# Kernel tuning notes

Measured on AMD Instinct MI355X. Metric: run time of the kernel, lower is better.

The kernel has to match this reference:

```python
import jax, jax.numpy as jnp
import numpy as np

B, S, D, H = 2, 2048, 1024, 16
DEPTH = D // H


def setup_inputs() -> dict:
    key = jax.random.key(0)
    ks = jax.random.split(key, 11)
    s = 1.0 / np.sqrt(D)
    return {
        "Q": jax.random.normal(ks[0], (B, S, D), jnp.float32),
        "K": jax.random.normal(ks[1], (B, S, D), jnp.float32),
        "V": jax.random.normal(ks[2], (B, S, D), jnp.float32),
        "wq": jax.random.normal(ks[3], (D, D), jnp.float32) * s,
        "bq": jnp.zeros((D,), jnp.float32),
        "wk": jax.random.normal(ks[4], (D, D), jnp.float32) * s,
        "bk": jnp.zeros((D,), jnp.float32),
        "wv": jax.random.normal(ks[5], (D, D), jnp.float32) * s,
        "bv": jnp.zeros((D,), jnp.float32),
        "wo": jax.random.normal(ks[6], (D, D), jnp.float32) * s,
        "bo": jnp.zeros((D,), jnp.float32),
    }


def _split_heads(x):
    # [B, S, D] -> [B, H, S, depth]
    b, s, _ = x.shape
    return x.reshape(b, s, H, DEPTH).transpose(0, 2, 1, 3)


def reference(Q, K, V, wq, bq, wk, bk, wv, bv, wo, bo):
    q = _split_heads(Q @ wq + bq)
    k = _split_heads(K @ wk + bk)
    v = _split_heads(V @ wv + bv)
    scores = jnp.einsum("bhqd,bhkd->bhqk", q, k) / jnp.sqrt(jnp.float32(DEPTH))
    weights = jax.nn.softmax(scores, axis=-1)
    attn = jnp.einsum("bhqk,bhkd->bhqd", weights, v)
    concat = attn.transpose(0, 2, 1, 3).reshape(Q.shape[0], -1, D)
    out = concat @ wo + bo
    return out, weights
```

## Files before the change

kernel.cpp:

```cpp
#include <hip/hip_runtime.h>
#include <stdint.h>


typedef _Float16 half8 __attribute__((ext_vector_type(8)));
typedef float f32x4 __attribute__((ext_vector_type(4)));

#define MFMA16(a, b, c) __builtin_amdgcn_mfma_f32_16x16x32_f16((a), (b), (c), 0, 0, 0)

__device__ __forceinline__ void load_lds16(const void* g, void* l) {
  __builtin_amdgcn_global_load_lds(
      (const __attribute__((address_space(1))) void*)(uintptr_t)g,
      (__attribute__((address_space(3))) void*)(uintptr_t)l, 16, 0, 0);
}

__global__ __launch_bounds__(256) void cvt_f16_kernel(
    const float* __restrict__ i0, const float* __restrict__ i1,
    const float* __restrict__ i2, _Float16* __restrict__ o0,
    _Float16* __restrict__ o1, _Float16* __restrict__ o2) {
  const float* in;
  _Float16* out;
  switch (blockIdx.y) {
    case 0: in = i0; out = o0; break;
    case 1: in = i1; out = o1; break;
    default: in = i2; out = o2; break;
  }
  const int i = blockIdx.x * 256 + threadIdx.x;
  const float4* p = (const float4*)in + 2 * (size_t)i;
  float4 a = p[0], b = p[1];
  half8 h;
  h[0] = (_Float16)a.x; h[1] = (_Float16)a.y; h[2] = (_Float16)a.z; h[3] = (_Float16)a.w;
  h[4] = (_Float16)b.x; h[5] = (_Float16)b.y; h[6] = (_Float16)b.z; h[7] = (_Float16)b.w;
  *((half8*)out + i) = h;
}

__global__ __launch_bounds__(256) void transpose_cvt_kernel(
    const float* __restrict__ i0, const float* __restrict__ i1,
    const float* __restrict__ i2, const float* __restrict__ i3,
    _Float16* __restrict__ o0, _Float16* __restrict__ o1,
    _Float16* __restrict__ o2, _Float16* __restrict__ o3) {
  const float* in;
  _Float16* out;
  switch (blockIdx.z) {
    case 0: in = i0; out = o0; break;
    case 1: in = i1; out = o1; break;
    case 2: in = i2; out = o2; break;
    default: in = i3; out = o3; break;
  }
  __shared__ _Float16 tile[64][72];
  const int r  = threadIdx.x >> 2;
  const int c4 = threadIdx.x & 3;
  const int kin = blockIdx.y * 64, nin = blockIdx.x * 64;
#pragma unroll
  for (int i = 0; i < 4; ++i) {
    float4 v = *(const float4*)(in + (size_t)(kin + r) * 1024 + nin + c4 * 16 + i * 4);
    tile[c4 * 16 + i * 4 + 0][r] = (_Float16)v.x;
    tile[c4 * 16 + i * 4 + 1][r] = (_Float16)v.y;
    tile[c4 * 16 + i * 4 + 2][r] = (_Float16)v.z;
    tile[c4 * 16 + i * 4 + 3][r] = (_Float16)v.w;
  }
  __syncthreads();
#pragma unroll
  for (int i = 0; i < 4; ++i) {
    union { _Float16 hh[4]; uint2 u; } p;
    p.hh[0] = tile[r][c4 * 16 + i * 4 + 0];
    p.hh[1] = tile[r][c4 * 16 + i * 4 + 1];
    p.hh[2] = tile[r][c4 * 16 + i * 4 + 2];
    p.hh[3] = tile[r][c4 * 16 + i * 4 + 3];
    *(uint2*)(out + (size_t)(nin + r) * 1024 + kin + c4 * 16 + i * 4) = p.u;
  }
}

struct GemmArgs {
  const _Float16* A[3];
  const _Float16* BT[3];
  const float* bias[3];
  void* out[3];
};

__global__ __launch_bounds__(256, 3) void gemm_f16_kernel(GemmArgs ga, int K,
                                                          int modes) {
  const _Float16* __restrict__ A  = ga.A[blockIdx.z];
  const _Float16* __restrict__ BT = ga.BT[blockIdx.z];
  const float* __restrict__ bias  = ga.bias[blockIdx.z];
  void* __restrict__ out          = ga.out[blockIdx.z];
  const int MODE = (modes >> (4 * blockIdx.z)) & 15;

  __shared__ __align__(16) _Float16 As[128 * 32];
  __shared__ __align__(16) _Float16 Bs[128 * 32];
  const int tid = threadIdx.x;
  const int w = tid >> 6, l = tid & 63;
  const int g = l >> 4, c = l & 15;
  const int tm = blockIdx.y * 128, tn = blockIdx.x * 128;
  const int wr = w >> 1, wc = w & 1;

  f32x4 acc[4][4];
#pragma unroll
  for (int i = 0; i < 4; ++i)
#pragma unroll
    for (int j = 0; j < 4; ++j) acc[i][j] = (f32x4){0.f, 0.f, 0.f, 0.f};

  const int srow0 = w * 16 + (l >> 2);
  const int sl = l & 3;

  for (int kt = 0; kt < K; kt += 32) {
#pragma unroll
    for (int r = 0; r < 2; ++r) {
      const int row = r * 64 + srow0;
      const int kc = sl ^ ((row >> 1) & 3);
      load_lds16(A + (size_t)(tm + row) * K + kt + kc * 8, As + row * 32 + sl * 8);
      load_lds16(BT + (size_t)(tn + row) * K + kt + kc * 8, Bs + row * 32 + sl * 8);
    }
    __syncthreads();
    half8 af[4], bf[4];
#pragma unroll
    for (int mt = 0; mt < 4; ++mt) {
      const int row = wr * 64 + mt * 16 + c;
      af[mt] = *(const half8*)(As + row * 32 + (g ^ ((row >> 1) & 3)) * 8);
    }
#pragma unroll
    for (int nt = 0; nt < 4; ++nt) {
      const int row = wc * 64 + nt * 16 + c;
      bf[nt] = *(const half8*)(Bs + row * 32 + (g ^ ((row >> 1) & 3)) * 8);
    }
#pragma unroll
    for (int mt = 0; mt < 4; ++mt)
#pragma unroll
      for (int nt = 0; nt < 4; ++nt)
        acc[mt][nt] = MFMA16(af[mt], bf[nt], acc[mt][nt]);
    __syncthreads();
  }

#pragma unroll
  for (int mt = 0; mt < 4; ++mt) {
#pragma unroll
    for (int nt = 0; nt < 4; ++nt) {
      const int n = tn + wc * 64 + nt * 16 + c;
      const float bv = bias[n];
      if (MODE == 2) {
#pragma unroll
        for (int r = 0; r < 4; ++r) {
          const int m = tm + wr * 64 + mt * 16 + 4 * g + r;
          ((float*)out)[(size_t)m * 1024 + n] = acc[mt][nt][r] + bv;
        }
      } else if (MODE == 0) {
        const int h_ = n >> 6, d_ = n & 63;
#pragma unroll
        for (int r = 0; r < 4; ++r) {
          const int m = tm + wr * 64 + mt * 16 + 4 * g + r;
          const int b_ = m >> 11, s_ = m & 2047;
          ((_Float16*)out)[((size_t)(b_ * 16 + h_) * 2048 + s_) * 64 + d_] =
              (_Float16)(acc[mt][nt][r] + bv);
        }
      } else {
        const int h_ = n >> 6, d_ = n & 63;
        const int m0 = tm + wr * 64 + mt * 16 + 4 * g;
        const int b_ = m0 >> 11, s0 = m0 & 2047;
        union { _Float16 hh[4]; uint2 u; } p;
#pragma unroll
        for (int r = 0; r < 4; ++r) p.hh[r] = (_Float16)(acc[mt][nt][r] + bv);
        *(uint2*)((_Float16*)out + ((size_t)(b_ * 16 + h_) * 64 + d_) * 2048 + s0) = p.u;
      }
    }
  }
}

__global__ __launch_bounds__(256, 2) void pv_kernel(
    const _Float16* __restrict__ qh,
    const _Float16* __restrict__ kh,
    const _Float16* __restrict__ vT,
    float* __restrict__ invp,
    _Float16* __restrict__ concat) {
  __shared__ __align__(16) char arena[32768];
  _Float16* Kb0 = (_Float16*)(arena);
  _Float16* Kb1 = (_Float16*)(arena + 8192);
  _Float16* Vb0 = (_Float16*)(arena + 16384);
  _Float16* Vb1 = (_Float16*)(arena + 24576);

  const int tid = threadIdx.x;
  const int w = tid >> 6, l = tid & 63;
  const int g = l >> 4, c = l & 15;
  const int qt = blockIdx.x, h = blockIdx.y, b = blockIdx.z;
  const int bh = b * 16 + h;
  const int q0 = qt * 128 + w * 32;
  const _Float16* qp = qh + ((size_t)bh * 2048 + q0) * 64;
  const _Float16* kp = kh + (size_t)bh * 2048 * 64;
  const _Float16* vp = vT + (size_t)bh * 64 * 2048;

  const half8 aq00 = *(const half8*)(qp + (size_t)c * 64 + 8 * g);
  const half8 aq01 = *(const half8*)(qp + (size_t)c * 64 + 32 + 8 * g);
  const half8 aq10 = *(const half8*)(qp + (size_t)(16 + c) * 64 + 8 * g);
  const half8 aq11 = *(const half8*)(qp + (size_t)(16 + c) * 64 + 32 + 8 * g);

  f32x4 pvA0 = {0,0,0,0}, pvA1 = {0,0,0,0}, pvA2 = {0,0,0,0}, pvA3 = {0,0,0,0};
  f32x4 pvB0 = {0,0,0,0}, pvB1 = {0,0,0,0}, pvB2 = {0,0,0,0}, pvB3 = {0,0,0,0};
  float sum0 = 0.f, sum1 = 0.f;

  const int L01 = (2 * (g & 1)) * 16 + c;
  const int L23 = L01 + 16;
  const bool lohalf = (g < 2);

  const int n0 = tid, n1 = tid + 256;
  const int r0 = n0 >> 3, s0 = n0 & 7, z0 = (s0 ^ (r0 & 7)) * 8;
  const int r1 = n1 >> 3, s1 = n1 & 7, z1 = (s1 ^ (r1 & 7)) * 8;

#define STAGE_PV(Kb, Vb, kc)                                                 \
  do {                                                                       \
    load_lds16(kp + (size_t)((kc) + r0) * 64 + z0, (Kb) + n0 * 8);           \
    load_lds16(kp + (size_t)((kc) + r1) * 64 + z1, (Kb) + n1 * 8);           \
    load_lds16(vp + (size_t)r0 * 2048 + (kc) + z0, (Vb) + n0 * 8);           \
    load_lds16(vp + (size_t)r1 * 2048 + (kc) + z1, (Vb) + n1 * 8);           \
  } while (0)

  STAGE_PV(Kb0, Vb0, 0);
  __syncthreads();

#pragma unroll 1
  for (int ch = 0; ch < 32; ++ch) {
    const int cur = ch & 1;
    const _Float16* Kb = cur ? Kb1 : Kb0;
    const _Float16* Vb = cur ? Vb1 : Vb0;
    if (ch < 31) {
      if (cur) STAGE_PV(Kb0, Vb0, (ch + 1) * 64);
      else     STAGE_PV(Kb1, Vb1, (ch + 1) * 64);
    }

    float e0[16], e1[16];
#pragma unroll
    for (int t = 0; t < 4; ++t) {
      const int krow = t * 16 + c;
      const int swz = krow & 7;
      half8 k0 = *(const half8*)(Kb + krow * 64 + ((g ^ swz) * 8));
      half8 k1 = *(const half8*)(Kb + krow * 64 + (((4 + g) ^ swz) * 8));
      f32x4 sA = {0.f, 0.f, 0.f, 0.f}, sB = {0.f, 0.f, 0.f, 0.f};
      sA = MFMA16(k0, aq00, sA);
      sA = MFMA16(k1, aq01, sA);
      sB = MFMA16(k0, aq10, sB);
      sB = MFMA16(k1, aq11, sB);
#pragma unroll
      for (int r = 0; r < 4; ++r) {
        e0[t * 4 + r] = __expf(sA[r] * 0.125f);
        sum0 += e0[t * 4 + r];
        e1[t * 4 + r] = __expf(sB[r] * 0.125f);
        sum1 += e1[t * 4 + r];
      }
    }

#pragma unroll
    for (int kh2 = 0; kh2 < 2; ++kh2) {
      const int d0 = 0 * 16 + c, d1 = 1 * 16 + c, d2 = 2 * 16 + c, d3 = 3 * 16 + c;
      half8 v0 = *(const half8*)(Vb + d0 * 64 + (((kh2 * 4 + g) ^ (d0 & 7)) * 8));
      half8 v1 = *(const half8*)(Vb + d1 * 64 + (((kh2 * 4 + g) ^ (d1 & 7)) * 8));
      half8 v2 = *(const half8*)(Vb + d2 * 64 + (((kh2 * 4 + g) ^ (d2 & 7)) * 8));
      half8 v3 = *(const half8*)(Vb + d3 * 64 + (((kh2 * 4 + g) ^ (d3 & 7)) * 8));

      {
        union { _Float16 h2[2]; unsigned u; } p0, p1, p2, p3;
        p0.h2[0] = (_Float16)e0[kh2*8+0]; p0.h2[1] = (_Float16)e0[kh2*8+1];
        p1.h2[0] = (_Float16)e0[kh2*8+2]; p1.h2[1] = (_Float16)e0[kh2*8+3];
        p2.h2[0] = (_Float16)e0[kh2*8+4]; p2.h2[1] = (_Float16)e0[kh2*8+5];
        p3.h2[0] = (_Float16)e0[kh2*8+6]; p3.h2[1] = (_Float16)e0[kh2*8+7];
        unsigned s0a = __shfl(p0.u, L01, 64), s0b = __shfl(p2.u, L01, 64);
        unsigned s1a = __shfl(p1.u, L01, 64), s1b = __shfl(p3.u, L01, 64);
        unsigned s2a = __shfl(p0.u, L23, 64), s2b = __shfl(p2.u, L23, 64);
        unsigned s3a = __shfl(p1.u, L23, 64), s3b = __shfl(p3.u, L23, 64);
        union { unsigned u[4]; half8 h; } aw;
        aw.u[0] = lohalf ? s0a : s0b;
        aw.u[1] = lohalf ? s1a : s1b;
        aw.u[2] = lohalf ? s2a : s2b;
        aw.u[3] = lohalf ? s3a : s3b;
        pvA0 = MFMA16(aw.h, v0, pvA0);
        pvA1 = MFMA16(aw.h, v1, pvA1);
        pvA2 = MFMA16(aw.h, v2, pvA2);
        pvA3 = MFMA16(aw.h, v3, pvA3);
      }
      {
        union { _Float16 h2[2]; unsigned u; } p0, p1, p2, p3;
        p0.h2[0] = (_Float16)e1[kh2*8+0]; p0.h2[1] = (_Float16)e1[kh2*8+1];
        p1.h2[0] = (_Float16)e1[kh2*8+2]; p1.h2[1] = (_Float16)e1[kh2*8+3];
        p2.h2[0] = (_Float16)e1[kh2*8+4]; p2.h2[1] = (_Float16)e1[kh2*8+5];
        p3.h2[0] = (_Float16)e1[kh2*8+6]; p3.h2[1] = (_Float16)e1[kh2*8+7];
        unsigned s0a = __shfl(p0.u, L01, 64), s0b = __shfl(p2.u, L01, 64);
        unsigned s1a = __shfl(p1.u, L01, 64), s1b = __shfl(p3.u, L01, 64);
        unsigned s2a = __shfl(p0.u, L23, 64), s2b = __shfl(p2.u, L23, 64);
        unsigned s3a = __shfl(p1.u, L23, 64), s3b = __shfl(p3.u, L23, 64);
        union { unsigned u[4]; half8 h; } aw;
        aw.u[0] = lohalf ? s0a : s0b;
        aw.u[1] = lohalf ? s1a : s1b;
        aw.u[2] = lohalf ? s2a : s2b;
        aw.u[3] = lohalf ? s3a : s3b;
        pvB0 = MFMA16(aw.h, v0, pvB0);
        pvB1 = MFMA16(aw.h, v1, pvB1);
        pvB2 = MFMA16(aw.h, v2, pvB2);
        pvB3 = MFMA16(aw.h, v3, pvB3);
      }
    }
    __syncthreads();
  }
#undef STAGE_PV

  sum0 += __shfl_xor(sum0, 16, 64);
  sum0 += __shfl_xor(sum0, 32, 64);
  sum1 += __shfl_xor(sum1, 16, 64);
  sum1 += __shfl_xor(sum1, 32, 64);
  const float inv0 = 1.0f / sum0;
  const float inv1 = 1.0f / sum1;
  if (l < 16) {
    invp[(size_t)bh * 2048 + q0 + l] = inv0;
    invp[(size_t)bh * 2048 + q0 + 16 + l] = inv1;
  }
  float ivA[4], ivB[4];
#pragma unroll
  for (int r = 0; r < 4; ++r) {
    ivA[r] = __shfl(inv0, 4 * g + r, 64);
    ivB[r] = __shfl(inv1, 4 * g + r, 64);
  }

  float* part = (float*)arena + w * (16 * 68);
  const int ql = l & 15, dh2 = l >> 4;
#pragma unroll
  for (int qs = 0; qs < 2; ++qs) {
    const f32x4* s0p = qs ? &pvB0 : &pvA0;
    const f32x4* s1p = qs ? &pvB1 : &pvA1;
    const f32x4* s2p = qs ? &pvB2 : &pvA2;
    const f32x4* s3p = qs ? &pvB3 : &pvA3;
    const float* iv = qs ? ivB : ivA;
#pragma unroll
    for (int r = 0; r < 4; ++r) {
      part[(4 * g + r) * 68 + 0 * 16 + c] = (*s0p)[r] * iv[r];
      part[(4 * g + r) * 68 + 1 * 16 + c] = (*s1p)[r] * iv[r];
      part[(4 * g + r) * 68 + 2 * 16 + c] = (*s2p)[r] * iv[r];
      part[(4 * g + r) * 68 + 3 * 16 + c] = (*s3p)[r] * iv[r];
    }
    __builtin_amdgcn_s_waitcnt(0);
    union { _Float16 hh[8]; uint4 u4; } pk;
#pragma unroll
    for (int half = 0; half < 2; ++half) {
#pragma unroll
      for (int i = 0; i < 8; ++i)
        pk.hh[i] = (_Float16)part[ql * 68 + dh2 * 16 + half * 8 + i];
      *(uint4*)(concat + (size_t)(b * 2048 + q0 + qs * 16 + ql) * 1024 +
                h * 64 + dh2 * 16 + half * 8) = pk.u4;
    }
  }
}

__global__ __launch_bounds__(256, 2) void wts_kernel(
    const _Float16* __restrict__ qh, const _Float16* __restrict__ kh,
    const float* __restrict__ invp, float* __restrict__ wout) {
  __shared__ __align__(16) _Float16 Qs[128 * 64];
  __shared__ __align__(16) _Float16 Ks[128 * 64];
  __shared__ __align__(16) float stg[4][16][132];
  __shared__ float invs[128];
  const int tid = threadIdx.x;
  const int w = tid >> 6, l = tid & 63;
  const int g = l >> 4, c = l & 15;
  const int tk = blockIdx.x * 128, tq = blockIdx.y * 128;
  const int bh = blockIdx.z;
  const _Float16* qg = qh + ((size_t)bh * 2048 + tq) * 64;
  const _Float16* kg = kh + ((size_t)bh * 2048 + tk) * 64;

  if (tid < 128) invs[tid] = invp[(size_t)bh * 2048 + tq + tid];

#pragma unroll
  for (int rnd = 0; rnd < 4; ++rnd) {
    const int seg = w * 4 + rnd;
    const int row = seg * 8 + (l >> 3);
    const int ss = (l & 7) ^ (row & 7);
    load_lds16(qg + (size_t)row * 64 + ss * 8, Qs + seg * 512 + l * 8);
    load_lds16(kg + (size_t)row * 64 + ss * 8, Ks + seg * 512 + l * 8);
  }
  __syncthreads();

  half8 af[2][2];
#pragma unroll
  for (int mt = 0; mt < 2; ++mt) {
#pragma unroll
    for (int dh = 0; dh < 2; ++dh) {
      const int row = w * 32 + mt * 16 + c;
      af[mt][dh] = *(const half8*)(Qs + row * 64 + (((dh * 4 + g) ^ (row & 7)) * 8));
    }
  }

  f32x4 acc[2][8];
#pragma unroll
  for (int mt = 0; mt < 2; ++mt)
#pragma unroll
    for (int nt = 0; nt < 8; ++nt) acc[mt][nt] = (f32x4){0.f, 0.f, 0.f, 0.f};

#pragma unroll
  for (int nt = 0; nt < 8; ++nt) {
    const int row = nt * 16 + c;
    half8 bf0 = *(const half8*)(Ks + row * 64 + ((g ^ (row & 7)) * 8));
    half8 bf1 = *(const half8*)(Ks + row * 64 + (((4 + g) ^ (row & 7)) * 8));
    acc[0][nt] = MFMA16(af[0][0], bf0, acc[0][nt]);
    acc[0][nt] = MFMA16(af[0][1], bf1, acc[0][nt]);
    acc[1][nt] = MFMA16(af[1][0], bf0, acc[1][nt]);
    acc[1][nt] = MFMA16(af[1][1], bf1, acc[1][nt]);
  }

#pragma unroll
  for (int hs = 0; hs < 2; ++hs) {
#pragma unroll
    for (int r = 0; r < 4; ++r) {
      const float iv = invs[w * 32 + hs * 16 + 4 * g + r];
#pragma unroll
      for (int nt = 0; nt < 8; ++nt)
        stg[w][4 * g + r][nt * 16 + c] = __expf(acc[hs][nt][r] * 0.125f) * iv;
    }
    asm volatile("s_waitcnt lgkmcnt(0)" ::: "memory");
#pragma unroll
    for (int i = 0; i < 8; ++i) {
      const int idx = i * 64 + l;
      const int row = idx >> 5, col4 = idx & 31;
      f32x4 v = *(const f32x4*)(&stg[w][row][col4 * 4]);
      __builtin_nontemporal_store(
          v, (f32x4*)(wout + ((size_t)bh * 2048 + tq + w * 32 + hs * 16 + row) *
                                 2048 + tk) + col4);
    }
  }
}

extern "C" void kernel_launch(void* const* d_in, const int* in_sizes, int n_in,
                              void* d_out, int out_size, void* d_ws, size_t ws_size,
                              hipStream_t stream) {
  const float* Q  = (const float*)d_in[0];
  const float* Kx = (const float*)d_in[1];
  const float* V  = (const float*)d_in[2];
  const float* wq = (const float*)d_in[3];
  const float* bq = (const float*)d_in[4];
  const float* wk = (const float*)d_in[5];
  const float* bk = (const float*)d_in[6];
  const float* wv = (const float*)d_in[7];
  const float* bv = (const float*)d_in[8];
  const float* wo = (const float*)d_in[9];
  const float* bo = (const float*)d_in[10];

  float* out  = (float*)d_out;
  float* wout = out + (size_t)4194304;

  char* ws = (char*)d_ws;
  const size_t MB = 1024 * 1024;
  _Float16* Xq  = (_Float16*)(ws + 0 * MB);
  _Float16* Xk  = (_Float16*)(ws + 8 * MB);
  _Float16* Xv  = (_Float16*)(ws + 16 * MB);
  _Float16* wqT = (_Float16*)(ws + 24 * MB);
  _Float16* wkT = (_Float16*)(ws + 26 * MB);
  _Float16* wvT = (_Float16*)(ws + 28 * MB);
  _Float16* woT = (_Float16*)(ws + 30 * MB);
  _Float16* qhp = (_Float16*)(ws + 32 * MB);
  _Float16* khp = (_Float16*)(ws + 40 * MB);
  _Float16* vTp = (_Float16*)(ws + 48 * MB);
  _Float16* cat = (_Float16*)(ws + 56 * MB);
  float*    invp = (float*)(ws + 16 * MB);

  cvt_f16_kernel<<<dim3(2048, 3), 256, 0, stream>>>(Q, Kx, V, Xq, Xk, Xv);
  transpose_cvt_kernel<<<dim3(16, 16, 4), 256, 0, stream>>>(
      wq, wk, wv, wo, wqT, wkT, wvT, woT);

  GemmArgs qkv;
  qkv.A[0] = Xq;  qkv.A[1] = Xk;  qkv.A[2] = Xv;
  qkv.BT[0] = wqT; qkv.BT[1] = wkT; qkv.BT[2] = wvT;
  qkv.bias[0] = bq; qkv.bias[1] = bk; qkv.bias[2] = bv;
  qkv.out[0] = qhp; qkv.out[1] = khp; qkv.out[2] = vTp;
  gemm_f16_kernel<<<dim3(8, 32, 3), 256, 0, stream>>>(qkv, 1024, 0x100);

  pv_kernel<<<dim3(16, 16, 2), 256, 0, stream>>>(qhp, khp, vTp, invp, cat);
  wts_kernel<<<dim3(16, 16, 32), 256, 0, stream>>>(qhp, khp, invp, wout);

  GemmArgs og;
  og.A[0] = cat; og.A[1] = cat; og.A[2] = cat;
  og.BT[0] = woT; og.BT[1] = woT; og.BT[2] = woT;
  og.bias[0] = bo; og.bias[1] = bo; og.bias[2] = bo;
  og.out[0] = out; og.out[1] = out; og.out[2] = out;
  gemm_f16_kernel<<<dim3(8, 32, 1), 256, 0, stream>>>(og, 1024, 0x2);
}
```

Baseline: 241.5 us.

## Merge prologue conversions and fuse output projection into weights kernel launch

Merges the activation f16 conversion and the weight transpose-conversion into one prologue launch. It also folds the output-projection GEMM into the attention-weights kernel as an extra z-slice of blocks sharing one LDS arena. The goal is to cut launch overhead and let the output GEMM overlap with the large weights-writing work instead of running as a serialized tail. In exchange, both block types in the fused kernel share one LDS footprint and occupancy limit, which may constrain the GEMM blocks.

```diff
diff --git a/kernel.cpp b/kernel.cpp
--- a/kernel.cpp
+++ b/kernel.cpp
@@ -13,43 +13,45 @@
       (__attribute__((address_space(3))) void*)(uintptr_t)l, 16, 0, 0);
 }
 
-__global__ __launch_bounds__(256) void cvt_f16_kernel(
-    const float* __restrict__ i0, const float* __restrict__ i1,
-    const float* __restrict__ i2, _Float16* __restrict__ o0,
-    _Float16* __restrict__ o1, _Float16* __restrict__ o2) {
+__global__ __launch_bounds__(256) void prologue_kernel(
+    const float* __restrict__ Q, const float* __restrict__ K,
+    const float* __restrict__ V, _Float16* __restrict__ Xq,
+    _Float16* __restrict__ Xk, _Float16* __restrict__ Xv,
+    const float* __restrict__ wq, const float* __restrict__ wk,
+    const float* __restrict__ wv, const float* __restrict__ wo,
+    _Float16* __restrict__ wqT, _Float16* __restrict__ wkT,
+    _Float16* __restrict__ wvT, _Float16* __restrict__ woT) {
+  __shared__ _Float16 tile[64][72];
+  const int bid = blockIdx.x;
+  if (bid < 6144) {
+    const float* in;
+    _Float16* out;
+    const int which = bid >> 11;
+    if (which == 0) { in = Q; out = Xq; }
+    else if (which == 1) { in = K; out = Xk; }
+    else { in = V; out = Xv; }
+    const int i = (bid & 2047) * 256 + threadIdx.x;
+    const float4* p = (const float4*)in + 2 * (size_t)i;
+    float4 a = p[0], b = p[1];
+    half8 h;
+    h[0] = (_Float16)a.x; h[1] = (_Float16)a.y; h[2] = (_Float16)a.z; h[3] = (_Float16)a.w;
+    h[4] = (_Float16)b.x; h[5] = (_Float16)b.y; h[6] = (_Float16)b.z; h[7] = (_Float16)b.w;
+    *((half8*)out + i) = h;
+    return;
+  }
+  const int id2 = bid - 6144;
   const float* in;
   _Float16* out;
-  switch (blockIdx.y) {
-    case 0: in = i0; out = o0; break;
-    case 1: in = i1; out = o1; break;
-    default: in = i2; out = o2; break;
-  }
-  const int i = blockIdx.x * 256 + threadIdx.x;
-  const float4* p = (const float4*)in + 2 * (size_t)i;
-  float4 a = p[0], b = p[1];
-  half8 h;
-  h[0] = (_Float16)a.x; h[1] = (_Float16)a.y; h[2] = (_Float16)a.z; h[3] = (_Float16)a.w;
-  h[4] = (_Float16)b.x; h[5] = (_Float16)b.y; h[6] = (_Float16)b.z; h[7] = (_Float16)b.w;
-  *((half8*)out + i) = h;
-}
-
-__global__ __launch_bounds__(256) void transpose_cvt_kernel(
-    const float* __restrict__ i0, const float* __restrict__ i1,
-    const float* __restrict__ i2, const float* __restrict__ i3,
-    _Float16* __restrict__ o0, _Float16* __restrict__ o1,
-    _Float16* __restrict__ o2, _Float16* __restrict__ o3) {
-  const float* in;
-  _Float16* out;
-  switch (blockIdx.z) {
-    case 0: in = i0; out = o0; break;
-    case 1: in = i1; out = o1; break;
-    case 2: in = i2; out = o2; break;
-    default: in = i3; out = o3; break;
-  }
-  __shared__ _Float16 tile[64][72];
+  switch (id2 >> 8) {
+    case 0: in = wq; out = wqT; break;
+    case 1: in = wk; out = wkT; break;
+    case 2: in = wv; out = wvT; break;
+    default: in = wo; out = woT; break;
+  }
+  const int rem = id2 & 255;
+  const int nin = (rem & 15) * 64, kin = (rem >> 4) * 64;
   const int r  = threadIdx.x >> 2;
   const int c4 = threadIdx.x & 3;
-  const int kin = blockIdx.y * 64, nin = blockIdx.x * 64;
 #pragma unroll
   for (int i = 0; i < 4; ++i) {
     float4 v = *(const float4*)(in + (size_t)(kin + r) * 1024 + nin + c4 * 16 + i * 4);
@@ -136,13 +138,7 @@
     for (int nt = 0; nt < 4; ++nt) {
       const int n = tn + wc * 64 + nt * 16 + c;
       const float bv = bias[n];
-      if (MODE == 2) {
-#pragma unroll
-        for (int r = 0; r < 4; ++r) {
-          const int m = tm + wr * 64 + mt * 16 + 4 * g + r;
-          ((float*)out)[(size_t)m * 1024 + n] = acc[mt][nt][r] + bv;
-        }
-      } else if (MODE == 0) {
+      if (MODE == 0) {
         const int h_ = n >> 6, d_ = n & 63;
 #pragma unroll
         for (int r = 0; r < 4; ++r) {
@@ -344,18 +340,82 @@
   }
 }
 
-__global__ __launch_bounds__(256, 2) void wts_kernel(
+__global__ __launch_bounds__(256, 2) void wts_og_kernel(
     const _Float16* __restrict__ qh, const _Float16* __restrict__ kh,
-    const float* __restrict__ invp, float* __restrict__ wout) {
-  __shared__ __align__(16) _Float16 Qs[128 * 64];
-  __shared__ __align__(16) _Float16 Ks[128 * 64];
-  __shared__ __align__(16) float stg[4][16][132];
-  __shared__ float invs[128];
+    const float* __restrict__ invp, float* __restrict__ wout,
+    const _Float16* __restrict__ cat, const _Float16* __restrict__ woT,
+    const float* __restrict__ bo, float* __restrict__ outp) {
+  __shared__ __align__(16) char arena[67072];
   const int tid = threadIdx.x;
   const int w = tid >> 6, l = tid & 63;
   const int g = l >> 4, c = l & 15;
+
+  if (blockIdx.z == 0) {
+    _Float16* As = (_Float16*)arena;
+    _Float16* Bs = (_Float16*)(arena + 8192);
+    const int id = blockIdx.y * 16 + blockIdx.x;
+    const int tn = (id & 7) * 128, tm = (id >> 3) * 128;
+    const int wr = w >> 1, wc = w & 1;
+
+    f32x4 acc[4][4];
+#pragma unroll
+    for (int i = 0; i < 4; ++i)
+#pragma unroll
+      for (int j = 0; j < 4; ++j) acc[i][j] = (f32x4){0.f, 0.f, 0.f, 0.f};
+
+    const int srow0 = w * 16 + (l >> 2);
+    const int sl = l & 3;
+
+    for (int kt = 0; kt < 1024; kt += 32) {
+#pragma unroll
+      for (int r = 0; r < 2; ++r) {
+        const int row = r * 64 + srow0;
+        const int kc = sl ^ ((row >> 1) & 3);
+        load_lds16(cat + (size_t)(tm + row) * 1024 + kt + kc * 8, As + row * 32 + sl * 8);
+        load_lds16(woT + (size_t)(tn + row) * 1024 + kt + kc * 8, Bs + row * 32 + sl * 8);
+      }
+      __syncthreads();
+      half8 af[4], bf[4];
+#pragma unroll
+      for (int mt = 0; mt < 4; ++mt) {
+        const int row = wr * 64 + mt * 16 + c;
+        af[mt] = *(const half8*)(As + row * 32 + (g ^ ((row >> 1) & 3)) * 8);
+      }
+#pragma unroll
+      for (int nt = 0; nt < 4; ++nt) {
+        const int row = wc * 64 + nt * 16 + c;
+        bf[nt] = *(const half8*)(Bs + row * 32 + (g ^ ((row >> 1) & 3)) * 8);
+      }
+#pragma unroll
+      for (int mt = 0; mt < 4; ++mt)
+#pragma unroll
+        for (int nt = 0; nt < 4; ++nt)
+          acc[mt][nt] = MFMA16(af[mt], bf[nt], acc[mt][nt]);
+      __syncthreads();
+    }
+
+#pragma unroll
+    for (int mt = 0; mt < 4; ++mt) {
+#pragma unroll
+      for (int nt = 0; nt < 4; ++nt) {
+        const int n = tn + wc * 64 + nt * 16 + c;
+        const float bv = bo[n];
+#pragma unroll
+        for (int r = 0; r < 4; ++r) {
+          const int m = tm + wr * 64 + mt * 16 + 4 * g + r;
+          outp[(size_t)m * 1024 + n] = acc[mt][nt][r] + bv;
+        }
+      }
+    }
+    return;
+  }
+
+  _Float16* Qs = (_Float16*)arena;
+  _Float16* Ks = (_Float16*)(arena + 16384);
+  float (*stg)[16][132] = (float(*)[16][132])(arena + 32768);
+  float* invs = (float*)(arena + 66560);
   const int tk = blockIdx.x * 128, tq = blockIdx.y * 128;
-  const int bh = blockIdx.z;
+  const int bh = blockIdx.z - 1;
   const _Float16* qg = qh + ((size_t)bh * 2048 + tq) * 64;
   const _Float16* kg = kh + ((size_t)bh * 2048 + tk) * 64;
 
@@ -453,9 +513,8 @@
   _Float16* cat = (_Float16*)(ws + 56 * MB);
   float*    invp = (float*)(ws + 16 * MB);
 
-  cvt_f16_kernel<<<dim3(2048, 3), 256, 0, stream>>>(Q, Kx, V, Xq, Xk, Xv);
-  transpose_cvt_kernel<<<dim3(16, 16, 4), 256, 0, stream>>>(
-      wq, wk, wv, wo, wqT, wkT, wvT, woT);
+  prologue_kernel<<<7168, 256, 0, stream>>>(Q, Kx, V, Xq, Xk, Xv, wq, wk, wv,
+                                            wo, wqT, wkT, wvT, woT);
 
   GemmArgs qkv;
   qkv.A[0] = Xq;  qkv.A[1] = Xk;  qkv.A[2] = Xv;
@@ -465,12 +524,6 @@
   gemm_f16_kernel<<<dim3(8, 32, 3), 256, 0, stream>>>(qkv, 1024, 0x100);
 
   pv_kernel<<<dim3(16, 16, 2), 256, 0, stream>>>(qhp, khp, vTp, invp, cat);
-  wts_kernel<<<dim3(16, 16, 32), 256, 0, stream>>>(qhp, khp, invp, wout);
-
-  GemmArgs og;
-  og.A[0] = cat; og.A[1] = cat; og.A[2] = cat;
-  og.BT[0] = woT; og.BT[1] = woT; og.BT[2] = woT;
-  og.bias[0] = bo; og.bias[1] = bo; og.bias[2] = bo;
-  og.out[0] = out; og.out[1] = out; og.out[2] = out;
-  gemm_f16_kernel<<<dim3(8, 32, 1), 256, 0, stream>>>(og, 1024, 0x2);
+  wts_og_kernel<<<dim3(16, 16, 33), 256, 0, stream>>>(qhp, khp, invp, wout,
+                                                      cat, woT, bo, out);
 }
```

Result: faster. 226.3 us (-6.3%).
